# Kernel optimization log

Hardware: AMD Instinct MI355X
Metric: run time of the kernel (lower is better)

## Reference

```python
import jax, jax.numpy as jnp
import numpy as np

L, B, N = 2048, 128, 256
DT = 1.0 / L  # dt ~ 1/sequence_length per the docstring


def _hippo_legs(n):
    # transition('legs', n) from the original module
    q = np.arange(n, dtype=np.float64)
    col, row = np.meshgrid(q, q)
    r = 2 * q + 1
    M = -(np.where(row >= col, r, 0) - np.diag(q))
    T = np.sqrt(np.diag(2 * q + 1))
    A = T @ M @ np.linalg.inv(T)
    Bv = np.diag(T)  # (n,)
    return A, Bv


def _bilinear_discretize(A, Bv, dt):
    # scipy.signal.cont2discrete(..., method='bilinear')
    n = A.shape[0]
    I = np.eye(n)
    M = np.linalg.inv(I - (dt / 2.0) * A)
    dA = M @ (I + (dt / 2.0) * A)
    dB = (M @ (dt * Bv[:, None])).squeeze(-1)
    return dA, dB


def setup_inputs() -> dict:
    key = jax.random.key(0)
    A, Bv = _hippo_legs(N)
    dA, dB = _bilinear_discretize(A, Bv, DT)
    inputs = jax.random.normal(key, (L, B), dtype=jnp.float32)
    return {
        "inputs": inputs,
        "dA": jnp.asarray(dA, dtype=jnp.float32),
        "dB": jnp.asarray(dB, dtype=jnp.float32),
    }


def reference(inputs, dA, dB):
    # c_t = dA @ c_{t-1} + dB * f_t   (F.linear(c, dA) == c @ dA.T)
    n = dA.shape[0]
    c0 = jnp.zeros(inputs.shape[1:] + (n,), dtype=inputs.dtype)

    def step(c, f):
        c = c @ dA.T + f[..., None] * dB  # (B, N)
        return c, c

    _, cs = jax.lax.scan(step, c0, inputs)  # (L, B, N)
    return cs
```

## Files before the change

kernel.cpp:

```cpp
#include <hip/hip_runtime.h>
#include <hip/hip_cooperative_groups.h>
#include <stdint.h>
#include <stddef.h>

namespace cg = cooperative_groups;


typedef _Float16 f16;
typedef f16 half8 __attribute__((ext_vector_type(8)));
typedef float f32x4 __attribute__((ext_vector_type(4)));

#define SEQL 2048
#define NB 128
#define NS 256
#define PADROWS 64
#define LDA 72
#define LDB 72
#define LDC 280

#define SCAN0 56

__device__ __forceinline__ half8 h8zero() {
  half8 v;
#pragma unroll
  for (int u = 0; u < 8; u++) v[u] = (f16)0.f;
  return v;
}


__device__ __forceinline__ void stage_rows(f16* dst, int ld, int nrows,
                                           const f16* src, int sstride,
                                           int nvalid, int tid) {
  int tasks = nrows * 8;
  for (int i = tid; i < tasks; i += 512) {
    int row = i >> 3, c = (i & 7) << 3;
    half8 v = h8zero();
    if (row < nvalid) v = *(const half8*)(src + (size_t)row * sstride + c);
    *(half8*)(dst + row * ld + (c ^ (row & 56))) = v;
  }
}

__device__ __forceinline__ void stage_rows32(f16* dst, int ld, int nrows,
                                             const float* src, int sstride, int tid) {
  int tasks = nrows * 8;
  for (int i = tid; i < tasks; i += 512) {
    int row = i >> 3, c = (i & 7) << 3;
    const float* p = src + (size_t)row * sstride + c;
    half8 v;
#pragma unroll
    for (int u = 0; u < 8; u++) v[u] = (f16)p[u];
    *(half8*)(dst + row * ld + (c ^ (row & 56))) = v;
  }
}

__device__ __forceinline__ void stage_revtrans(f16* As, const f16* xpad,
                                               int s_top, int s_min, int tid) {
  for (int i = tid; i < 1024; i += 512) {
    int q = i >> 4, bb = (i & 15) << 3;
    int s = s_top - q;
    half8 v = h8zero();
    if (s >= s_min) v = *(const half8*)(xpad + (size_t)(PADROWS + s) * NB + bb);
#pragma unroll
    for (int u = 0; u < 8; u++) {
      int row = bb + u;
      As[row * LDA + (q ^ (row & 56))] = v[u];
    }
  }
}


template <int NT>
struct RowsPrefetch {
  half8 v[NT];
  __device__ __forceinline__ void load(const f16* src, int sstride, int nvalid, int tid) {
#pragma unroll
    for (int j = 0; j < NT; j++) {
      int i = tid + j * 512;
      int row = i >> 3, c = (i & 7) << 3;
      v[j] = (row < nvalid) ? *(const half8*)(src + (size_t)row * sstride + c)
                            : h8zero();
    }
  }
  __device__ __forceinline__ void store(f16* dst, int ld, int tid) {
#pragma unroll
    for (int j = 0; j < NT; j++) {
      int i = tid + j * 512;
      int row = i >> 3, c = (i & 7) << 3;
      *(half8*)(dst + row * ld + (c ^ (row & 56))) = v[j];
    }
  }
};

template <int NT>
struct TransPrefetch {
  half8 v[NT];
  __device__ __forceinline__ void load(const f16* X, int c0, int tid) {
#pragma unroll
    for (int j = 0; j < NT; j++) {
      int i = tid + j * 512;
      int c = i >> 5, jj = (i & 31) << 3;
      v[j] = *(const half8*)(X + (size_t)(c0 + c) * NS + jj);
    }
  }
  __device__ __forceinline__ void store(f16* Bs, int tid) {
#pragma unroll
    for (int j = 0; j < NT; j++) {
      int i = tid + j * 512;
      int c = i >> 5, jj = (i & 31) << 3;
#pragma unroll
      for (int u = 0; u < 8; u++) {
        int row = jj + u;
        Bs[row * LDB + (c ^ (row & 56))] = v[j][u];
      }
    }
  }
};

__device__ __forceinline__ void mm64(const f16* As, const f16* Bs,
                                     f32x4 acc[4][4], int wm, int wn,
                                     int l15, int quad) {
#pragma unroll
  for (int ks = 0; ks < 64; ks += 32) {
    half8 a[4], b[4];
#pragma unroll
    for (int ms = 0; ms < 4; ms++) {
      int ar = wm * 64 + ms * 16 + l15;
      a[ms] = *(const half8*)(As + ar * LDA + ((ks + quad * 8) ^ (ar & 56)));
    }
#pragma unroll
    for (int ns = 0; ns < 4; ns++) {
      int br = wn * 64 + ns * 16 + l15;
      b[ns] = *(const half8*)(Bs + br * LDB + ((ks + quad * 8) ^ (br & 56)));
    }
#pragma unroll
    for (int ms = 0; ms < 4; ms++)
#pragma unroll
      for (int ns = 0; ns < 4; ns++)
        acc[ms][ns] = __builtin_amdgcn_mfma_f32_16x16x32_f16(a[ms], b[ns], acc[ms][ns], 0, 0, 0);
  }
}

__device__ __forceinline__ void acc_zero(f32x4 acc[4][4]) {
#pragma unroll
  for (int ms = 0; ms < 4; ms++)
#pragma unroll
    for (int ns = 0; ns < 4; ns++)
#pragma unroll
      for (int u = 0; u < 4; u++) acc[ms][ns][u] = 0.f;
}

__device__ __forceinline__ void acc_store_split(const f32x4 acc[4][4], f16* H, f16* L,
                                                int rowoff, int wm, int wn, int l15, int quad) {
#pragma unroll
  for (int ms = 0; ms < 4; ms++)
#pragma unroll
    for (int ns = 0; ns < 4; ns++)
#pragma unroll
      for (int u = 0; u < 4; u++) {
        int row = rowoff + wm * 64 + ms * 16 + quad * 4 + u;
        int col = wn * 64 + ns * 16 + l15;
        float v = acc[ms][ns][u];
        f16 h = (f16)v;
        H[(size_t)row * NS + col] = h;
        L[(size_t)row * NS + col] = (f16)(v - (float)h);
      }
}

__device__ __forceinline__ void acc_store_f32(const f32x4 acc[4][4], float* dst,
                                              int wm, int wn, int l15, int quad) {
#pragma unroll
  for (int ms = 0; ms < 4; ms++)
#pragma unroll
    for (int ns = 0; ns < 4; ns++)
#pragma unroll
      for (int u = 0; u < 4; u++)
        dst[(size_t)(wm * 64 + ms * 16 + quad * 4 + u) * NS +
            wn * 64 + ns * 16 + l15] = acc[ms][ns][u];
}

__device__ __forceinline__ void product_split_pipe(const f16* AH, const f16* AL,
                                                   const f16* BH, const f16* BL,
                                                   f16* DH, f16* DL, int mtile,
                                                   f16* As, f16* Bs,
                                                   int tid, int wm, int wn,
                                                   int l15, int quad) {
  f32x4 acc[4][4];
  acc_zero(acc);
  RowsPrefetch<2> ap;
  TransPrefetch<4> bp;
  const size_t arow = (size_t)(mtile * 128) * NS;
  ap.load(AL + arow, NS, 128, tid);
  bp.load(BH, 0, tid);
  ap.store(As, LDA, tid);
  bp.store(Bs, tid);
  __syncthreads();
#pragma unroll 1
  for (int s = 0; s < 12; s++) {
    int sn = s + 1;
    int restA = 0, restB = 0;
    if (sn < 12) {
      int c3 = sn % 3, ccn = sn / 3;
      if (c3 == 0) {
        ap.load(AL + arow + ccn * 64, NS, 128, tid);
        bp.load(BH, ccn * 64, tid);
        restA = restB = 1;
      } else if (c3 == 1) {
        ap.load(AH + arow + ccn * 64, NS, 128, tid);
        restA = 1;
      } else {
        bp.load(BL, ccn * 64, tid);
        restB = 1;
      }
    }
    mm64(As, Bs, acc, wm, wn, l15, quad);
    __syncthreads();
    if (restA) ap.store(As, LDA, tid);
    if (restB) bp.store(Bs, tid);
    __syncthreads();
  }
  acc_store_split(acc, DH, DL, mtile * 128, wm, wn, l15, quad);
}

__global__ void __launch_bounds__(512)
k_setup(const float* __restrict__ x, const float* __restrict__ dA,
        const float* __restrict__ dB,
        f16* __restrict__ PrH, f16* __restrict__ PrL,
        f16* __restrict__ Kt, f16* __restrict__ xpad,
        float* __restrict__ V0, float* __restrict__ V1) {
  cg::grid_group grid = cg::this_grid();
  __shared__ alignas(16) f16 As[128 * LDA];
  __shared__ alignas(16) f16 Bs[256 * LDB];
  __shared__ float dBs[NS];
  int tid = threadIdx.x;
  int lane = tid & 63, wid = tid >> 6;
  int wm = wid >> 2, wn = wid & 3;
  int l15 = lane & 15, quad = lane >> 4;
  int bi = blockIdx.x;

  {
    const int XPN = (PADROWS + SEQL) * NB;
    for (int g = bi * 512 + tid; g < XPN; g += 64 * 512) {
      int s = g >> 7;
      xpad[g] = (s < PADROWS) ? (f16)0.f : (f16)x[g - PADROWS * NB];
    }
    for (int g = bi * 512 + tid; g < NS * NS; g += 64 * 512) {
      float v = dA[g];
      f16 h = (f16)v;
      PrH[g] = h;
      PrL[g] = (f16)(v - (float)h);
    }
  }
  grid.sync();

#pragma unroll 1
  for (int m = 1; m <= 32; m <<= 1) {
    if (bi < 2 * m) {
      int prod = bi >> 1, mtile = bi & 1, r = prod + 1;
      product_split_pipe(PrH + (size_t)(m - 1) * 65536, PrL + (size_t)(m - 1) * 65536,
                         PrH + (size_t)(r - 1) * 65536, PrL + (size_t)(r - 1) * 65536,
                         PrH + (size_t)(m + r - 1) * 65536, PrL + (size_t)(m + r - 1) * 65536,
                         mtile, As, Bs, tid, wm, wn, l15, quad);
    }
    grid.sync();
  }

  {
    if (tid < NS) dBs[tid] = dB[tid];
    __syncthreads();
    int j = bi;
    if (tid < NS) {
      int n = tid;
      float a;
      if (j == 0) {
        a = dBs[n];
      } else {
        const f16* rh = PrH + (size_t)(j - 1) * 65536 + (size_t)n * NS;
        const f16* rl = PrL + (size_t)(j - 1) * 65536 + (size_t)n * NS;
        a = 0.f;
#pragma unroll 4
        for (int c = 0; c < NS; c += 8) {
          half8 vh = *(const half8*)(rh + c);
          half8 vl = *(const half8*)(rl + c);
#pragma unroll
          for (int u = 0; u < 8; u++) a += ((float)vh[u] + (float)vl[u]) * dBs[c + u];
        }
      }
      Kt[(size_t)n * 64 + j] = (f16)a;
    }
  }
  grid.sync();

  if (bi < 31) {
    int k = bi, t = 64 * k + 63;
    f32x4 acc[4][4];
    acc_zero(acc);
    stage_revtrans(As, xpad, t, 64 * k, tid);
    stage_rows(Bs, LDB, 256, Kt, 64, 256, tid);
    __syncthreads();
    mm64(As, Bs, acc, wm, wn, l15, quad);
    __syncthreads();
    acc_store_f32(acc, V0 + (size_t)k * 32768, wm, wn, l15, quad);
  }
  grid.sync();

  if (bi >= SCAN0) {
    int s = bi - SCAN0;
    int w = wid;
    const f16* SH = PrH + (size_t)63 * 65536;
    const f16* SL = PrL + (size_t)63 * 65536;
    half8 sfh[2][8], sfl[2][8];
#pragma unroll
    for (int nt = 0; nt < 2; nt++) {
      int n = (w * 2 + nt) * 16 + l15;
#pragma unroll
      for (int ks2 = 0; ks2 < 8; ks2++) {
        sfh[nt][ks2] = *(const half8*)(SH + (size_t)n * NS + ks2 * 32 + quad * 8);
        sfl[nt][ks2] = *(const half8*)(SL + (size_t)n * NS + ks2 * 32 + quad * 8);
      }
    }
    f16* Chi = As;
    f16* Clo = As + 16 * LDC;
    f32x4 acc2[2];
#pragma unroll 1
    for (int k = 0; k < 31; k++) {
#pragma unroll
      for (int nt = 0; nt < 2; nt++) {
        int col = (w * 2 + nt) * 16 + l15;
#pragma unroll
        for (int u = 0; u < 4; u++)
          acc2[nt][u] = V0[(size_t)k * 32768 + (size_t)(s * 16 + quad * 4 + u) * NS + col];
      }
      if (k > 0) {
#pragma unroll
        for (int ks2 = 0; ks2 < 8; ks2++) {
          half8 ah = *(const half8*)(Chi + l15 * LDC + ks2 * 32 + quad * 8);
          half8 al = *(const half8*)(Clo + l15 * LDC + ks2 * 32 + quad * 8);
#pragma unroll
          for (int nt = 0; nt < 2; nt++) {
            acc2[nt] = __builtin_amdgcn_mfma_f32_16x16x32_f16(ah, sfh[nt][ks2], acc2[nt], 0, 0, 0);
            acc2[nt] = __builtin_amdgcn_mfma_f32_16x16x32_f16(al, sfh[nt][ks2], acc2[nt], 0, 0, 0);
            acc2[nt] = __builtin_amdgcn_mfma_f32_16x16x32_f16(ah, sfl[nt][ks2], acc2[nt], 0, 0, 0);
          }
        }
      }
      __syncthreads();
#pragma unroll
      for (int nt = 0; nt < 2; nt++) {
        int col = (w * 2 + nt) * 16 + l15;
#pragma unroll
        for (int u = 0; u < 4; u++) {
          int row = quad * 4 + u;
          float v = acc2[nt][u];
          f16 h = (f16)v;
          Chi[row * LDC + col] = h;
          Clo[row * LDC + col] = (f16)(v - (float)h);
          V1[(size_t)k * 32768 + (size_t)(s * 16 + row) * NS + col] = v;
        }
      }
      __syncthreads();
    }
  }
}

__global__ void __launch_bounds__(512, 4)
k_pass2(const f16* __restrict__ PrH, const f16* __restrict__ Kt,
        const f16* __restrict__ xpad, const float* __restrict__ Vfin,
        float* __restrict__ out) {
  __shared__ alignas(16) f16 As[128 * LDA];
  __shared__ alignas(16) f16 Bs[256 * LDB];
  int tid = threadIdx.x;
  int lane = tid & 63, wid = tid >> 6;
  int wm = wid >> 2, wn = wid & 3;
  int l15 = lane & 15, quad = lane >> 4;
  int bi = blockIdx.x;
  int r = bi >> 5, k = bi & 31;
  int t = 64 * k + r;
  const f16* G = PrH + (size_t)r * 65536;
  f32x4 acc[4][4];
  acc_zero(acc);
  if (k > 0) {
    const float* C = Vfin + (size_t)(k - 1) * 32768;
    RowsPrefetch<4> bp;
    bp.load(G, NS, 256, tid);
    stage_rows32(As, LDA, 128, C, NS, tid);
    bp.store(Bs, LDB, tid);
    __syncthreads();
#pragma unroll 1
    for (int cc = 0; cc < 4; cc++) {
      if (cc < 3) bp.load(G + (cc + 1) * 64, NS, 256, tid);
      else        bp.load(Kt, 64, 256, tid);
      mm64(As, Bs, acc, wm, wn, l15, quad);
      __syncthreads();
      bp.store(Bs, LDB, tid);
      if (cc < 3) stage_rows32(As, LDA, 128, C + (cc + 1) * 64, NS, tid);
      else        stage_revtrans(As, xpad, t, 64 * k, tid);
      __syncthreads();
    }
    mm64(As, Bs, acc, wm, wn, l15, quad);
  } else {
    stage_revtrans(As, xpad, t, 64 * k, tid);
    stage_rows(Bs, LDB, 256, Kt, 64, 256, tid);
    __syncthreads();
    mm64(As, Bs, acc, wm, wn, l15, quad);
  }
  acc_store_f32(acc, out + (size_t)t * (NB * NS), wm, wn, l15, quad);
}

extern "C" void kernel_launch(void* const* d_in, const int* in_sizes, int n_in,
                              void* d_out, int out_size, void* d_ws, size_t ws_size,
                              hipStream_t stream) {
  const float* x = (const float*)d_in[0];
  const float* dA = (const float*)d_in[1];
  const float* dB = (const float*)d_in[2];
  float* out = (float*)d_out;

  char* ws = (char*)d_ws;
  f16* PrH = (f16*)(ws + 0);
  f16* PrL = (f16*)(ws + 8388608);
  f16* Kt  = (f16*)(ws + 17825792);
  f16* Xp  = (f16*)(ws + 17858560);
  float* V0 = (float*)(ws + 18399232);
  float* V1 = (float*)(ws + 22462464);

  void* args[] = {&x, &dA, &dB, &PrH, &PrL, &Kt, &Xp, &V0, &V1};
  hipLaunchCooperativeKernel(reinterpret_cast<void*>(k_setup), dim3(64), dim3(512),
                             args, 0, stream);
  k_pass2<<<2048, 512, 0, stream>>>(PrH, Kt, Xp, V1, out);
}
```

Baseline: 616.7 us.

## Use unpadded swizzled LDS tiles, double-buffer A in split product, simplify pass2

Measured after the change: 634.3 us. 2.9% more time.

```diff
diff --git a/kernel.cpp b/kernel.cpp
--- a/kernel.cpp
+++ b/kernel.cpp
@@ -14,11 +14,12 @@
 #define NB 128
 #define NS 256
 #define PADROWS 64
-#define LDA 72
-#define LDB 72
+#define LD 64
 #define LDC 280
 
 #define SCAN0 56
+
+__device__ __forceinline__ int swz(int row) { return ((row ^ (row >> 3)) & 7) << 3; }
 
 __device__ __forceinline__ half8 h8zero() {
   half8 v;
@@ -28,7 +29,7 @@
 }
 
 
-__device__ __forceinline__ void stage_rows(f16* dst, int ld, int nrows,
+__device__ __forceinline__ void stage_rows(f16* dst, int nrows,
                                            const f16* src, int sstride,
                                            int nvalid, int tid) {
   int tasks = nrows * 8;
@@ -36,11 +37,11 @@
     int row = i >> 3, c = (i & 7) << 3;
     half8 v = h8zero();
     if (row < nvalid) v = *(const half8*)(src + (size_t)row * sstride + c);
-    *(half8*)(dst + row * ld + (c ^ (row & 56))) = v;
-  }
-}
-
-__device__ __forceinline__ void stage_rows32(f16* dst, int ld, int nrows,
+    *(half8*)(dst + row * LD + (c ^ swz(row))) = v;
+  }
+}
+
+__device__ __forceinline__ void stage_rows32(f16* dst, int nrows,
                                              const float* src, int sstride, int tid) {
   int tasks = nrows * 8;
   for (int i = tid; i < tasks; i += 512) {
@@ -49,7 +50,7 @@
     half8 v;
 #pragma unroll
     for (int u = 0; u < 8; u++) v[u] = (f16)p[u];
-    *(half8*)(dst + row * ld + (c ^ (row & 56))) = v;
+    *(half8*)(dst + row * LD + (c ^ swz(row))) = v;
   }
 }
 
@@ -63,7 +64,7 @@
 #pragma unroll
     for (int u = 0; u < 8; u++) {
       int row = bb + u;
-      As[row * LDA + (q ^ (row & 56))] = v[u];
+      As[row * LD + (q ^ swz(row))] = v[u];
     }
   }
 }
@@ -81,12 +82,12 @@
                             : h8zero();
     }
   }
-  __device__ __forceinline__ void store(f16* dst, int ld, int tid) {
+  __device__ __forceinline__ void store(f16* dst, int tid) {
 #pragma unroll
     for (int j = 0; j < NT; j++) {
       int i = tid + j * 512;
       int row = i >> 3, c = (i & 7) << 3;
-      *(half8*)(dst + row * ld + (c ^ (row & 56))) = v[j];
+      *(half8*)(dst + row * LD + (c ^ swz(row))) = v[j];
     }
   }
 };
@@ -110,7 +111,7 @@
 #pragma unroll
       for (int u = 0; u < 8; u++) {
         int row = jj + u;
-        Bs[row * LDB + (c ^ (row & 56))] = v[j][u];
+        Bs[row * LD + (c ^ swz(row))] = v[j][u];
       }
     }
   }
@@ -125,12 +126,12 @@
 #pragma unroll
     for (int ms = 0; ms < 4; ms++) {
       int ar = wm * 64 + ms * 16 + l15;
-      a[ms] = *(const half8*)(As + ar * LDA + ((ks + quad * 8) ^ (ar & 56)));
+      a[ms] = *(const half8*)(As + ar * LD + ((ks + quad * 8) ^ swz(ar)));
     }
 #pragma unroll
     for (int ns = 0; ns < 4; ns++) {
       int br = wn * 64 + ns * 16 + l15;
-      b[ns] = *(const half8*)(Bs + br * LDB + ((ks + quad * 8) ^ (br & 56)));
+      b[ns] = *(const half8*)(Bs + br * LD + ((ks + quad * 8) ^ swz(br)));
     }
 #pragma unroll
     for (int ms = 0; ms < 4; ms++)
@@ -178,45 +179,51 @@
             wn * 64 + ns * 16 + l15] = acc[ms][ns][u];
 }
 
-__device__ __forceinline__ void product_split_pipe(const f16* AH, const f16* AL,
-                                                   const f16* BH, const f16* BL,
-                                                   f16* DH, f16* DL, int mtile,
-                                                   f16* As, f16* Bs,
-                                                   int tid, int wm, int wn,
-                                                   int l15, int quad) {
+__device__ __forceinline__ void product_split_v2(const f16* AH, const f16* AL,
+                                                 const f16* BH, const f16* BL,
+                                                 f16* DH, f16* DL, int mtile,
+                                                 f16* AsD, f16* Bs,
+                                                 int tid, int wm, int wn,
+                                                 int l15, int quad) {
   f32x4 acc[4][4];
   acc_zero(acc);
   RowsPrefetch<2> ap;
   TransPrefetch<4> bp;
   const size_t arow = (size_t)(mtile * 128) * NS;
+  f16* A0 = AsD;
+  f16* A1 = AsD + 128 * LD;
+  bp.load(BH, 0, tid);
   ap.load(AL + arow, NS, 128, tid);
-  bp.load(BH, 0, tid);
-  ap.store(As, LDA, tid);
   bp.store(Bs, tid);
+  ap.store(A0, tid);
   __syncthreads();
+  int ab = 0;
 #pragma unroll 1
-  for (int s = 0; s < 12; s++) {
-    int sn = s + 1;
-    int restA = 0, restB = 0;
-    if (sn < 12) {
-      int c3 = sn % 3, ccn = sn / 3;
-      if (c3 == 0) {
-        ap.load(AL + arow + ccn * 64, NS, 128, tid);
-        bp.load(BH, ccn * 64, tid);
-        restA = restB = 1;
-      } else if (c3 == 1) {
-        ap.load(AH + arow + ccn * 64, NS, 128, tid);
-        restA = 1;
-      } else {
-        bp.load(BL, ccn * 64, tid);
-        restB = 1;
-      }
-    }
-    mm64(As, Bs, acc, wm, wn, l15, quad);
-    __syncthreads();
-    if (restA) ap.store(As, LDA, tid);
-    if (restB) bp.store(Bs, tid);
-    __syncthreads();
+  for (int cc = 0; cc < 4; cc++) {
+    f16* Acur = ab ? A1 : A0;
+    f16* Anxt = ab ? A0 : A1;
+    ap.load(AH + arow + cc * 64, NS, 128, tid);
+    mm64(Acur, Bs, acc, wm, wn, l15, quad);
+    ap.store(Anxt, tid);
+    __syncthreads();
+    ab ^= 1;
+    Acur = ab ? A1 : A0;
+    Anxt = ab ? A0 : A1;
+    bp.load(BL, cc * 64, tid);
+    mm64(Acur, Bs, acc, wm, wn, l15, quad);
+    __syncthreads();
+    bp.store(Bs, tid);
+    if (cc < 3) ap.load(AL + arow + (cc + 1) * 64, NS, 128, tid);
+    __syncthreads();
+    if (cc < 3) bp.load(BH, (cc + 1) * 64, tid);
+    mm64(Acur, Bs, acc, wm, wn, l15, quad);
+    if (cc < 3) {
+      ap.store(Anxt, tid);
+      __syncthreads();
+      bp.store(Bs, tid);
+      __syncthreads();
+      ab ^= 1;
+    }
   }
   acc_store_split(acc, DH, DL, mtile * 128, wm, wn, l15, quad);
 }
@@ -228,9 +235,8 @@
         f16* __restrict__ Kt, f16* __restrict__ xpad,
         float* __restrict__ V0, float* __restrict__ V1) {
   cg::grid_group grid = cg::this_grid();
-  __shared__ alignas(16) f16 As[128 * LDA];
-  __shared__ alignas(16) f16 Bs[256 * LDB];
-  __shared__ float dBs[NS];
+  __shared__ alignas(16) f16 AsD[2 * 128 * LD];
+  __shared__ alignas(16) f16 BsS[256 * LD];
   int tid = threadIdx.x;
   int lane = tid & 63, wid = tid >> 6;
   int wm = wid >> 2, wn = wid & 3;
@@ -256,15 +262,16 @@
   for (int m = 1; m <= 32; m <<= 1) {
     if (bi < 2 * m) {
       int prod = bi >> 1, mtile = bi & 1, r = prod + 1;
-      product_split_pipe(PrH + (size_t)(m - 1) * 65536, PrL + (size_t)(m - 1) * 65536,
-                         PrH + (size_t)(r - 1) * 65536, PrL + (size_t)(r - 1) * 65536,
-                         PrH + (size_t)(m + r - 1) * 65536, PrL + (size_t)(m + r - 1) * 65536,
-                         mtile, As, Bs, tid, wm, wn, l15, quad);
+      product_split_v2(PrH + (size_t)(m - 1) * 65536, PrL + (size_t)(m - 1) * 65536,
+                       PrH + (size_t)(r - 1) * 65536, PrL + (size_t)(r - 1) * 65536,
+                       PrH + (size_t)(m + r - 1) * 65536, PrL + (size_t)(m + r - 1) * 65536,
+                       mtile, AsD, BsS, tid, wm, wn, l15, quad);
     }
     grid.sync();
   }
 
   {
+    float* dBs = (float*)AsD;
     if (tid < NS) dBs[tid] = dB[tid];
     __syncthreads();
     int j = bi;
@@ -294,10 +301,10 @@
     int k = bi, t = 64 * k + 63;
     f32x4 acc[4][4];
     acc_zero(acc);
-    stage_revtrans(As, xpad, t, 64 * k, tid);
-    stage_rows(Bs, LDB, 256, Kt, 64, 256, tid);
-    __syncthreads();
-    mm64(As, Bs, acc, wm, wn, l15, quad);
+    stage_revtrans(AsD, xpad, t, 64 * k, tid);
+    stage_rows(BsS, 256, Kt, 64, 256, tid);
+    __syncthreads();
+    mm64(AsD, BsS, acc, wm, wn, l15, quad);
     __syncthreads();
     acc_store_f32(acc, V0 + (size_t)k * 32768, wm, wn, l15, quad);
   }
@@ -318,8 +325,8 @@
         sfl[nt][ks2] = *(const half8*)(SL + (size_t)n * NS + ks2 * 32 + quad * 8);
       }
     }
-    f16* Chi = As;
-    f16* Clo = As + 16 * LDC;
+    f16* Chi = AsD;
+    f16* Clo = AsD + 16 * LDC;
     f32x4 acc2[2];
 #pragma unroll 1
     for (int k = 0; k < 31; k++) {
@@ -362,12 +369,11 @@
   }
 }
 
-__global__ void __launch_bounds__(512, 4)
-k_pass2(const f16* __restrict__ PrH, const f16* __restrict__ Kt,
-        const f16* __restrict__ xpad, const float* __restrict__ Vfin,
-        float* __restrict__ out) {
-  __shared__ alignas(16) f16 As[128 * LDA];
-  __shared__ alignas(16) f16 Bs[256 * LDB];
+__global__ void k_pass2(const f16* __restrict__ PrH, const f16* __restrict__ Kt,
+                        const f16* __restrict__ xpad, const float* __restrict__ Vfin,
+                        float* __restrict__ out) {
+  __shared__ alignas(16) f16 As[128 * LD];
+  __shared__ alignas(16) f16 Bs[256 * LD];
   int tid = threadIdx.x;
   int lane = tid & 63, wid = tid >> 6;
   int wm = wid >> 2, wn = wid & 3;
@@ -380,29 +386,19 @@
   acc_zero(acc);
   if (k > 0) {
     const float* C = Vfin + (size_t)(k - 1) * 32768;
-    RowsPrefetch<4> bp;
-    bp.load(G, NS, 256, tid);
-    stage_rows32(As, LDA, 128, C, NS, tid);
-    bp.store(Bs, LDB, tid);
-    __syncthreads();
 #pragma unroll 1
     for (int cc = 0; cc < 4; cc++) {
-      if (cc < 3) bp.load(G + (cc + 1) * 64, NS, 256, tid);
-      else        bp.load(Kt, 64, 256, tid);
+      stage_rows32(As, 128, C + cc * 64, NS, tid);
+      stage_rows(Bs, 256, G + cc * 64, NS, 256, tid);
+      __syncthreads();
       mm64(As, Bs, acc, wm, wn, l15, quad);
       __syncthreads();
-      bp.store(Bs, LDB, tid);
-      if (cc < 3) stage_rows32(As, LDA, 128, C + (cc + 1) * 64, NS, tid);
-      else        stage_revtrans(As, xpad, t, 64 * k, tid);
-      __syncthreads();
-    }
-    mm64(As, Bs, acc, wm, wn, l15, quad);
-  } else {
-    stage_revtrans(As, xpad, t, 64 * k, tid);
-    stage_rows(Bs, LDB, 256, Kt, 64, 256, tid);
-    __syncthreads();
-    mm64(As, Bs, acc, wm, wn, l15, quad);
-  }
+    }
+  }
+  stage_revtrans(As, xpad, t, 64 * k, tid);
+  stage_rows(Bs, 256, Kt, 64, 256, tid);
+  __syncthreads();
+  mm64(As, Bs, acc, wm, wn, l15, quad);
   acc_store_f32(acc, out + (size_t)t * (NB * NS), wm, wn, l15, quad);
 }
 
```

## Use unpadded XOR-swizzled LDS tiles and drop register prefetch in pass2

Applied to the files above, without the earlier changes.

After: 604.0 us. -2.1%, faster.

```diff
diff --git a/kernel.cpp b/kernel.cpp
--- a/kernel.cpp
+++ b/kernel.cpp
@@ -16,6 +16,7 @@
 #define PADROWS 64
 #define LDA 72
 #define LDB 72
+#define LDP 64
 #define LDC 280
 
 #define SCAN0 56
@@ -40,19 +41,6 @@
   }
 }
 
-__device__ __forceinline__ void stage_rows32(f16* dst, int ld, int nrows,
-                                             const float* src, int sstride, int tid) {
-  int tasks = nrows * 8;
-  for (int i = tid; i < tasks; i += 512) {
-    int row = i >> 3, c = (i & 7) << 3;
-    const float* p = src + (size_t)row * sstride + c;
-    half8 v;
-#pragma unroll
-    for (int u = 0; u < 8; u++) v[u] = (f16)p[u];
-    *(half8*)(dst + row * ld + (c ^ (row & 56))) = v;
-  }
-}
-
 __device__ __forceinline__ void stage_revtrans(f16* As, const f16* xpad,
                                                int s_top, int s_min, int tid) {
   for (int i = tid; i < 1024; i += 512) {
@@ -68,7 +56,6 @@
   }
 }
 
-
 template <int NT>
 struct RowsPrefetch {
   half8 v[NT];
@@ -139,6 +126,74 @@
         acc[ms][ns] = __builtin_amdgcn_mfma_f32_16x16x32_f16(a[ms], b[ns], acc[ms][ns], 0, 0, 0);
   }
 }
+
+
+__device__ __forceinline__ int swz(int row) { return ((row ^ (row >> 3)) & 7) << 3; }
+
+__device__ __forceinline__ void stage_rows_s(f16* dst, int nrows,
+                                             const f16* src, int sstride,
+                                             int nvalid, int tid) {
+  int tasks = nrows * 8;
+  for (int i = tid; i < tasks; i += 512) {
+    int row = i >> 3, c = (i & 7) << 3;
+    half8 v = h8zero();
+    if (row < nvalid) v = *(const half8*)(src + (size_t)row * sstride + c);
+    *(half8*)(dst + row * LDP + (c ^ swz(row))) = v;
+  }
+}
+
+__device__ __forceinline__ void stage_rows32_s(f16* dst, int nrows,
+                                               const float* src, int sstride, int tid) {
+  int tasks = nrows * 8;
+  for (int i = tid; i < tasks; i += 512) {
+    int row = i >> 3, c = (i & 7) << 3;
+    const float* p = src + (size_t)row * sstride + c;
+    half8 v;
+#pragma unroll
+    for (int u = 0; u < 8; u++) v[u] = (f16)p[u];
+    *(half8*)(dst + row * LDP + (c ^ swz(row))) = v;
+  }
+}
+
+__device__ __forceinline__ void stage_revtrans_s(f16* As, const f16* xpad,
+                                                 int s_top, int s_min, int tid) {
+  for (int i = tid; i < 1024; i += 512) {
+    int q = i >> 4, bb = (i & 15) << 3;
+    int s = s_top - q;
+    half8 v = h8zero();
+    if (s >= s_min) v = *(const half8*)(xpad + (size_t)(PADROWS + s) * NB + bb);
+#pragma unroll
+    for (int u = 0; u < 8; u++) {
+      int row = bb + u;
+      As[row * LDP + (q ^ swz(row))] = v[u];
+    }
+  }
+}
+
+__device__ __forceinline__ void mm64_s(const f16* As, const f16* Bs,
+                                       f32x4 acc[4][4], int wm, int wn,
+                                       int l15, int quad) {
+#pragma unroll
+  for (int ks = 0; ks < 64; ks += 32) {
+    half8 a[4], b[4];
+#pragma unroll
+    for (int ms = 0; ms < 4; ms++) {
+      int ar = wm * 64 + ms * 16 + l15;
+      a[ms] = *(const half8*)(As + ar * LDP + ((ks + quad * 8) ^ swz(ar)));
+    }
+#pragma unroll
+    for (int ns = 0; ns < 4; ns++) {
+      int br = wn * 64 + ns * 16 + l15;
+      b[ns] = *(const half8*)(Bs + br * LDP + ((ks + quad * 8) ^ swz(br)));
+    }
+#pragma unroll
+    for (int ms = 0; ms < 4; ms++)
+#pragma unroll
+      for (int ns = 0; ns < 4; ns++)
+        acc[ms][ns] = __builtin_amdgcn_mfma_f32_16x16x32_f16(a[ms], b[ns], acc[ms][ns], 0, 0, 0);
+  }
+}
+
 
 __device__ __forceinline__ void acc_zero(f32x4 acc[4][4]) {
 #pragma unroll
@@ -362,12 +417,11 @@
   }
 }
 
-__global__ void __launch_bounds__(512, 4)
-k_pass2(const f16* __restrict__ PrH, const f16* __restrict__ Kt,
-        const f16* __restrict__ xpad, const float* __restrict__ Vfin,
-        float* __restrict__ out) {
-  __shared__ alignas(16) f16 As[128 * LDA];
-  __shared__ alignas(16) f16 Bs[256 * LDB];
+__global__ void k_pass2(const f16* __restrict__ PrH, const f16* __restrict__ Kt,
+                        const f16* __restrict__ xpad, const float* __restrict__ Vfin,
+                        float* __restrict__ out) {
+  __shared__ alignas(16) f16 As[128 * LDP];
+  __shared__ alignas(16) f16 Bs[256 * LDP];
   int tid = threadIdx.x;
   int lane = tid & 63, wid = tid >> 6;
   int wm = wid >> 2, wn = wid & 3;
@@ -380,29 +434,19 @@
   acc_zero(acc);
   if (k > 0) {
     const float* C = Vfin + (size_t)(k - 1) * 32768;
-    RowsPrefetch<4> bp;
-    bp.load(G, NS, 256, tid);
-    stage_rows32(As, LDA, 128, C, NS, tid);
-    bp.store(Bs, LDB, tid);
-    __syncthreads();
 #pragma unroll 1
     for (int cc = 0; cc < 4; cc++) {
-      if (cc < 3) bp.load(G + (cc + 1) * 64, NS, 256, tid);
-      else        bp.load(Kt, 64, 256, tid);
-      mm64(As, Bs, acc, wm, wn, l15, quad);
+      stage_rows32_s(As, 128, C + cc * 64, NS, tid);
+      stage_rows_s(Bs, 256, G + cc * 64, NS, 256, tid);
       __syncthreads();
-      bp.store(Bs, LDB, tid);
-      if (cc < 3) stage_rows32(As, LDA, 128, C + (cc + 1) * 64, NS, tid);
-      else        stage_revtrans(As, xpad, t, 64 * k, tid);
+      mm64_s(As, Bs, acc, wm, wn, l15, quad);
       __syncthreads();
     }
-    mm64(As, Bs, acc, wm, wn, l15, quad);
-  } else {
-    stage_revtrans(As, xpad, t, 64 * k, tid);
-    stage_rows(Bs, LDB, 256, Kt, 64, 256, tid);
-    __syncthreads();
-    mm64(As, Bs, acc, wm, wn, l15, quad);
-  }
+  }
+  stage_revtrans_s(As, xpad, t, 64 * k, tid);
+  stage_rows_s(Bs, 256, Kt, 64, 256, tid);
+  __syncthreads();
+  mm64_s(As, Bs, acc, wm, wn, l15, quad);
   acc_store_f32(acc, out + (size_t)t * (NB * NS), wm, wn, l15, quad);
 }
 
```
